# Performance work log

Measured on AMD Instinct MI355X. Metric: run time of the kernel, lower is better.

Reference implementation:

```python
import jax, jax.numpy as jnp
import numpy as np

N = 100_000      # nodes
E = 1_600_000    # directed edges (before self-loops)
F_IN = 256       # input node features
H = 128          # hidden_dim
HEADS = 2
C_HEAD = H // HEADS  # 64, GATConv out_channels per head
G = 128          # graphs in batch
NCLS = 10
NEG_SLOPE = 0.2  # PyG GATConv default


def setup_inputs() -> dict:
    key = jax.random.key(0)
    ks = jax.random.split(key, 20)
    p = lambda k, shape: (jax.random.normal(k, shape, jnp.float32) * 0.05)
    x = jax.random.normal(ks[0], (N, F_IN), jnp.float32)
    edge_index = jax.random.randint(ks[1], (2, E), 0, N, dtype=jnp.int64)
    batch = jnp.sort(jax.random.randint(ks[2], (N,), 0, G, dtype=jnp.int64))
    return dict(
        x=x, edge_index=edge_index, batch=batch,
        pre_w=p(ks[3], (F_IN, H)), pre_b=p(ks[4], (H,)),
        w1=p(ks[5], (H, H)), asrc1=p(ks[6], (HEADS, C_HEAD)), adst1=p(ks[7], (HEADS, C_HEAD)), b1=p(ks[8], (H,)),
        w2=p(ks[9], (H, H)), asrc2=p(ks[10], (HEADS, C_HEAD)), adst2=p(ks[11], (HEADS, C_HEAD)), b2=p(ks[12], (H,)),
        post_w1=p(ks[13], (H, H)), post_b1=p(ks[14], (H,)),
        post_w2=p(ks[15], (H, NCLS)), post_b2=p(ks[16], (NCLS,)),
    )


def _gat_conv(h_in, w, a_src, a_dst, b, src, dst):
    # h: [N, heads, c]
    h = (h_in @ w).reshape(N, HEADS, C_HEAD)
    alpha_src = jnp.sum(h * a_src, axis=-1)  # [N, heads]
    alpha_dst = jnp.sum(h * a_dst, axis=-1)  # [N, heads]
    e = jax.nn.leaky_relu(alpha_src[src] + alpha_dst[dst], NEG_SLOPE)  # [E+N, heads]
    # numerically stable softmax over incoming edges of each destination node
    m = jax.ops.segment_max(e, dst, num_segments=N)
    ex = jnp.exp(e - m[dst])
    denom = jax.ops.segment_sum(ex, dst, num_segments=N)
    alpha = ex / denom[dst]                                           # [E+N, heads]
    out = jax.ops.segment_sum(h[src] * alpha[:, :, None], dst, num_segments=N)
    return out.reshape(N, H) + b  # concat heads + bias


def reference(x, edge_index, batch, pre_w, pre_b,
              w1, asrc1, adst1, b1, w2, asrc2, adst2, b2,
              post_w1, post_b1, post_w2, post_b2):
    # PyG GATConv default add_self_loops=True
    loop = jnp.arange(N, dtype=edge_index.dtype)
    src = jnp.concatenate([edge_index[0], loop])
    dst = jnp.concatenate([edge_index[1], loop])

    h = jax.nn.relu(x @ pre_w + pre_b)
    reprs = jax.ops.segment_sum(h, batch, num_segments=G)
    h = jax.nn.relu(_gat_conv(h, w1, asrc1, adst1, b1, src, dst))
    reprs = reprs + jax.ops.segment_sum(h, batch, num_segments=G)
    h = jax.nn.relu(_gat_conv(h, w2, asrc2, adst2, b2, src, dst))
    reprs = reprs + jax.ops.segment_sum(h, batch, num_segments=G)
    z = jax.nn.relu(reprs @ post_w1 + post_b1) @ post_w2 + post_b2
    return jax.nn.log_softmax(z, axis=-1)
```

## Files before the change

### kernel.cpp

```cpp
#include <hip/hip_runtime.h>
#include <hip/hip_bf16.h>
#include <math.h>

#define NNODES 100000
#define NEDGES 1600000
#define FIN 256
#define HDIM 128
#define NGRAPH 128
#define NCLS 10
#define NEG 0.2f

#define NBUCK 98
#define EPB 4096
#define EBLK ((NEDGES + EPB - 1) / EPB)

typedef short bf8 __attribute__((ext_vector_type(8)));
typedef float f4 __attribute__((ext_vector_type(4)));

__device__ __forceinline__ float lrelu(float x) { return x > 0.f ? x : NEG * x; }

__device__ __forceinline__ unsigned short f2bf(float f) {
  union { float f; unsigned int u; } v; v.f = f;
  unsigned int r = v.u + 0x7fffu + ((v.u >> 16) & 1u);
  return (unsigned short)(r >> 16);
}
__device__ __forceinline__ float bf_lo(unsigned int p) {
  union { unsigned int u; float f; } v; v.u = p << 16; return v.f;
}
__device__ __forceinline__ float bf_hi(unsigned int p) {
  union { unsigned int u; float f; } v; v.u = p & 0xffff0000u; return v.f;
}

__global__ __launch_bounds__(256) void convert_transpose(const float* __restrict__ w,
                                                         unsigned short* __restrict__ wt,
                                                         int K) {
  int i = blockIdx.x * 256 + threadIdx.x;
  if (i >= K * 128) return;
  int k = i >> 7, n = i & 127;
  wt[n * K + k] = f2bf(w[(size_t)k * 128 + n]);
}

__global__ __launch_bounds__(256) void gemm_mfma(const float* __restrict__ A,
                                                 const unsigned short* __restrict__ Bt,
                                                 const float* __restrict__ bias,
                                                 float* __restrict__ C,
                                                 unsigned int* __restrict__ Cp,
                                                 const float* __restrict__ a_src,
                                                 const float* __restrict__ a_dst,
                                                 float* __restrict__ o_as,
                                                 float* __restrict__ o_ad,
                                                 int M, int K, int dorelu) {
  __shared__ bf8 As[512];
  __shared__ bf8 Bs[512];
  int tid = threadIdx.x;
  int wv = tid >> 6, lane = tid & 63;
  int quad = lane >> 4, m16 = lane & 15;
  int row0 = blockIdx.x * 128;

  f4 acc[2][8];
#pragma unroll
  for (int a = 0; a < 2; ++a)
#pragma unroll
    for (int b = 0; b < 8; ++b) acc[a][b] = (f4){0.f, 0.f, 0.f, 0.f};

  for (int kb = 0; kb < K; kb += 32) {
    __syncthreads();
#pragma unroll
    for (int bb = 0; bb < 2; ++bb) {
      int b = tid + bb * 256;
      int l = b & 63, mt = b >> 6;
      int row = row0 + mt * 16 + (l & 15);
      if (row > M - 1) row = M - 1;
      const float* src = &A[(size_t)row * K + kb + (l >> 4) * 8];
      float4 x0 = *reinterpret_cast<const float4*>(src);
      float4 x1 = *reinterpret_cast<const float4*>(src + 4);
      bf8 v;
      v[0] = (short)f2bf(x0.x); v[1] = (short)f2bf(x0.y);
      v[2] = (short)f2bf(x0.z); v[3] = (short)f2bf(x0.w);
      v[4] = (short)f2bf(x1.x); v[5] = (short)f2bf(x1.y);
      v[6] = (short)f2bf(x1.z); v[7] = (short)f2bf(x1.w);
      As[b] = v;
    }
#pragma unroll
    for (int bb = 0; bb < 2; ++bb) {
      int b = tid + bb * 256;
      int l = b & 63, tn = b >> 6;
      int n = tn * 16 + (l & 15);
      Bs[b] = *reinterpret_cast<const bf8*>(&Bt[(size_t)n * K + kb + (l >> 4) * 8]);
    }
    __syncthreads();
    bf8 af0 = As[(wv * 2 + 0) * 64 + lane];
    bf8 af1 = As[(wv * 2 + 1) * 64 + lane];
#pragma unroll
    for (int tn = 0; tn < 8; ++tn) {
      bf8 bfm = Bs[tn * 64 + lane];
      acc[0][tn] = __builtin_amdgcn_mfma_f32_16x16x32_bf16(af0, bfm, acc[0][tn], 0, 0, 0);
      acc[1][tn] = __builtin_amdgcn_mfma_f32_16x16x32_bf16(af1, bfm, acc[1][tn], 0, 0, 0);
    }
  }

  if (Cp) {
    if (a_src) {
      float aS[8], aD[8];
#pragma unroll
      for (int tn = 0; tn < 4; ++tn) {
        aS[tn]     = a_src[tn * 16 + m16];
        aS[tn + 4] = a_src[64 + tn * 16 + m16];
        aD[tn]     = a_dst[tn * 16 + m16];
        aD[tn + 4] = a_dst[64 + tn * 16 + m16];
      }
#pragma unroll
      for (int mt = 0; mt < 2; ++mt)
#pragma unroll
        for (int r = 0; r < 4; ++r) {
          int row = row0 + wv * 32 + mt * 16 + quad * 4 + r;
          float ps0 = 0.f, ps1 = 0.f, pd0 = 0.f, pd1 = 0.f;
#pragma unroll
          for (int tn = 0; tn < 4; ++tn) {
            float v0 = acc[mt][tn][r], v1 = acc[mt][tn + 4][r];
            ps0 = fmaf(v0, aS[tn], ps0);
            ps1 = fmaf(v1, aS[tn + 4], ps1);
            pd0 = fmaf(v0, aD[tn], pd0);
            pd1 = fmaf(v1, aD[tn + 4], pd1);
          }
#pragma unroll
          for (int o = 8; o; o >>= 1) {
            ps0 += __shfl_xor(ps0, o); ps1 += __shfl_xor(ps1, o);
            pd0 += __shfl_xor(pd0, o); pd1 += __shfl_xor(pd1, o);
          }
          if (m16 == 0 && row < M) {
            o_as[2 * row] = ps0; o_as[2 * row + 1] = ps1;
            o_ad[2 * row] = pd0; o_ad[2 * row + 1] = pd1;
          }
        }
    }
#pragma unroll
    for (int mt = 0; mt < 2; ++mt)
#pragma unroll
      for (int tn = 0; tn < 4; ++tn)
#pragma unroll
        for (int r = 0; r < 4; ++r) {
          int row = row0 + wv * 32 + mt * 16 + quad * 4 + r;
          if (row < M) {
            unsigned int p = (unsigned int)f2bf(acc[mt][tn][r]) |
                             ((unsigned int)f2bf(acc[mt][tn + 4][r]) << 16);
            Cp[(size_t)row * 64 + tn * 16 + m16] = p;
          }
        }
  } else {
#pragma unroll
    for (int mt = 0; mt < 2; ++mt)
#pragma unroll
      for (int tn = 0; tn < 8; ++tn) {
        float bv = bias ? bias[tn * 16 + m16] : 0.f;
#pragma unroll
        for (int r = 0; r < 4; ++r) {
          int row = row0 + wv * 32 + mt * 16 + quad * 4 + r;
          if (row < M) {
            float v = acc[mt][tn][r] + bv;
            if (dorelu) v = fmaxf(v, 0.f);
            C[(size_t)row * 128 + tn * 16 + m16] = v;
          }
        }
      }
  }
}

__global__ void find_starts(const int* __restrict__ batch, int* __restrict__ gstart) {
  int g = threadIdx.x;
  if (g > NGRAPH) return;
  if (g == NGRAPH) { gstart[g] = NNODES; return; }
  int lo = 0, hi = NNODES;
  while (lo < hi) { int mid = (lo + hi) >> 1; if (batch[mid] < g) lo = mid + 1; else hi = mid; }
  gstart[g] = lo;
}

__global__ __launch_bounds__(256) void bin_count(const int* __restrict__ edst,
                                                 int* __restrict__ blockHist) {
  __shared__ int hist[NBUCK];
  int t = threadIdx.x, blk = blockIdx.x;
  if (t < NBUCK) hist[t] = 0;
  __syncthreads();
  int e0 = blk * EPB;
#pragma unroll
  for (int it = 0; it < EPB / 256; ++it) {
    int e = e0 + it * 256 + t;
    if (e < NEDGES) atomicAdd(&hist[((unsigned)edst[e]) >> 10], 1);
  }
  __syncthreads();
  if (t < NBUCK) blockHist[blk * NBUCK + t] = hist[t];
}

__global__ __launch_bounds__(512) void colscan(const int* __restrict__ blockHist,
                                               int* __restrict__ blockBaseCol,
                                               int* __restrict__ bucket_total) {
  __shared__ int s[512];
  int b = blockIdx.x, t = threadIdx.x;
  int v = (t < EBLK) ? blockHist[t * NBUCK + b] : 0;
  s[t] = v;
  __syncthreads();
  for (int off = 1; off < 512; off <<= 1) {
    int u = (t >= off) ? s[t - off] : 0;
    __syncthreads();
    s[t] += u;
    __syncthreads();
  }
  if (t < EBLK) blockBaseCol[b * EBLK + t] = s[t] - v;
  if (t == 511) bucket_total[b] = s[511];
}

__global__ __launch_bounds__(128) void bscan(const int* __restrict__ bucket_total,
                                             int* __restrict__ bucket_ptr) {
  __shared__ int s[128];
  int t = threadIdx.x;
  int v = (t < NBUCK) ? bucket_total[t] : 0;
  s[t] = v;
  __syncthreads();
  for (int off = 1; off < 128; off <<= 1) {
    int u = (t >= off) ? s[t - off] : 0;
    __syncthreads();
    s[t] += u;
    __syncthreads();
  }
  if (t < NBUCK) bucket_ptr[t] = s[t] - v;
  if (t == 127) bucket_ptr[NBUCK] = s[127];
}

__global__ __launch_bounds__(512) void bin_place(const int* __restrict__ esrc,
                                                 const int* __restrict__ edst,
                                                 const int* __restrict__ blockBaseCol,
                                                 const int* __restrict__ bucket_ptr,
                                                 uint2* __restrict__ stagingG) {
  __shared__ int hist[NBUCK + 1], lbase[NBUCK + 1], lcur[NBUCK + 1], cbase[NBUCK];
  __shared__ int tmp[128];
  __shared__ uint2 st[EPB];
  int t = threadIdx.x, blk = blockIdx.x;
  if (t < NBUCK + 1) hist[t] = 0;
  __syncthreads();
  int e0 = blk * EPB;
#pragma unroll
  for (int it = 0; it < EPB / 512; ++it) {
    int e = e0 + it * 512 + t;
    int b = NBUCK;
    if (e < NEDGES) b = ((unsigned)edst[e]) >> 10;
    atomicAdd(&hist[b], 1);
  }
  __syncthreads();
  if (t < 128) tmp[t] = (t < NBUCK + 1) ? hist[t] : 0;
  __syncthreads();
  for (int off = 1; off < 128; off <<= 1) {
    int u = 0;
    if (t < 128 && t >= off) u = tmp[t - off];
    __syncthreads();
    if (t < 128) tmp[t] += u;
    __syncthreads();
  }
  if (t < NBUCK + 1) { int ex = tmp[t] - hist[t]; lbase[t] = ex; lcur[t] = ex; }
  if (t < NBUCK) cbase[t] = bucket_ptr[t] + blockBaseCol[t * EBLK + blk];
  __syncthreads();
#pragma unroll
  for (int it = 0; it < EPB / 512; ++it) {
    int e = e0 + it * 512 + t;
    unsigned s = 0, d = 0xFFFFFFFFu;
    if (e < NEDGES) { s = (unsigned)esrc[e]; d = (unsigned)edst[e]; }
    int b = (d == 0xFFFFFFFFu) ? NBUCK : (int)(d >> 10);
    int slot = atomicAdd(&lcur[b], 1);
    st[slot] = make_uint2(s, d);
  }
  __syncthreads();
  for (int i = t; i < EPB; i += 512) {
    uint2 ed = st[i];
    if (ed.y == 0xFFFFFFFFu) continue;
    int b = (int)(ed.y >> 10);
    stagingG[cbase[b] + (i - lbase[b])] = ed;
  }
}

__global__ __launch_bounds__(1024) void bucket_deg(const uint2* __restrict__ stagingG,
                                                   const int* __restrict__ bucket_ptr,
                                                   int* __restrict__ deg) {
  __shared__ int dl[1024];
  int b = blockIdx.x, t = threadIdx.x;
  dl[t] = 0;
  __syncthreads();
  int s0 = bucket_ptr[b], s1 = bucket_ptr[b + 1];
  for (int j = s0 + t; j < s1; j += 1024)
    atomicAdd(&dl[stagingG[j].y & 1023], 1);
  __syncthreads();
  int n = (b << 10) + t;
  if (n < NNODES) deg[n] = dl[t];
}

__global__ __launch_bounds__(256) void scan_block(const int* __restrict__ deg,
                                                  int* __restrict__ incl,
                                                  int* __restrict__ blocksum) {
  __shared__ int s[256];
  int tid = threadIdx.x;
  int i = blockIdx.x * 256 + tid;
  s[tid] = (i < NNODES) ? deg[i] : 0;
  __syncthreads();
  for (int off = 1; off < 256; off <<= 1) {
    int t = (tid >= off) ? s[tid - off] : 0;
    __syncthreads();
    s[tid] += t;
    __syncthreads();
  }
  if (i < NNODES) incl[i] = s[tid];
  if (tid == 255) blocksum[blockIdx.x] = s[255];
}

__global__ void scan_offsets(int* blocksum, int nb) {
  if (threadIdx.x == 0 && blockIdx.x == 0) {
    int run = 0;
    for (int b = 0; b < nb; ++b) { int t = blocksum[b]; blocksum[b] = run; run += t; }
  }
}

__global__ __launch_bounds__(256) void finalize_csr(const int* __restrict__ deg,
                                                    const int* __restrict__ incl,
                                                    const int* __restrict__ blocksum,
                                                    int* __restrict__ row_ptr) {
  int i = blockIdx.x * 256 + threadIdx.x;
  if (i >= NNODES) return;
  int tot = incl[i] + blocksum[i >> 8];
  row_ptr[i] = tot - deg[i];
  if (i == NNODES - 1) row_ptr[NNODES] = tot;
}

__global__ __launch_bounds__(1024) void bucket_csr(const uint2* __restrict__ stagingG,
                                                   const int* __restrict__ bucket_ptr,
                                                   const int* __restrict__ row_ptr,
                                                   int* __restrict__ colv) {
  __shared__ int cur[1024];
  int b = blockIdx.x, t = threadIdx.x;
  int n = (b << 10) + t;
  cur[t] = (n < NNODES) ? row_ptr[n] : 0;
  __syncthreads();
  int s0 = bucket_ptr[b], s1 = bucket_ptr[b + 1];
  for (int j = s0 + t; j < s1; j += 1024) {
    uint2 e = stagingG[j];
    int pos = atomicAdd(&cur[e.y & 1023], 1);
    colv[pos] = (int)e.x;
  }
}

template<int T>
__device__ __forceinline__ void gather_T(const unsigned int* __restrict__ hwb,
                                         int lane, int sl, float w0l, float w1l,
                                         float& acc0, float& acc1) {
#pragma unroll
  for (int t = 0; t < T; ++t) {
    int s = __builtin_amdgcn_readlane(sl, t);
    float w0 = __uint_as_float(__builtin_amdgcn_readlane(__float_as_uint(w0l), t));
    float w1 = __uint_as_float(__builtin_amdgcn_readlane(__float_as_uint(w1l), t));
    unsigned q = hwb[(size_t)s * 64 + lane];
    acc0 = fmaf(w0, bf_lo(q), acc0);
    acc1 = fmaf(w1, bf_hi(q), acc1);
  }
}

__global__ __launch_bounds__(256) void aggregate(const unsigned int* __restrict__ hwb,
                                                 const float* __restrict__ a_s,
                                                 const float* __restrict__ a_d,
                                                 const int* __restrict__ row_ptr,
                                                 const int* __restrict__ colv,
                                                 const float* __restrict__ bias,
                                                 float* __restrict__ out) {
  int i = (blockIdx.x * 256 + threadIdx.x) >> 6;
  int lane = threadIdx.x & 63;
  if (i >= NNODES) return;
  float ad0 = a_d[2 * i], ad1 = a_d[2 * i + 1];
  float es0 = lrelu(a_s[2 * i] + ad0), es1 = lrelu(a_s[2 * i + 1] + ad1);
  int start = row_ptr[i], end = row_ptr[i + 1];
  int deg = end - start;

  int sl = 0; float e0l = -1e30f, e1l = -1e30f;
  if (lane < deg) {
    sl = colv[start + lane];
    float2 av = *reinterpret_cast<const float2*>(&a_s[2 * sl]);
    e0l = lrelu(av.x + ad0); e1l = lrelu(av.y + ad1);
  }
  float m0 = fmaxf(es0, e0l), m1 = fmaxf(es1, e1l);
  for (int j = start + 64 + lane; j < end; j += 64) {
    int s = colv[j];
    float2 av = *reinterpret_cast<const float2*>(&a_s[2 * s]);
    m0 = fmaxf(m0, lrelu(av.x + ad0));
    m1 = fmaxf(m1, lrelu(av.y + ad1));
  }
  for (int o = 32; o; o >>= 1) {
    m0 = fmaxf(m0, __shfl_xor(m0, o));
    m1 = fmaxf(m1, __shfl_xor(m1, o));
  }
  float w0l = lane < deg ? __expf(e0l - m0) : 0.f;
  float w1l = lane < deg ? __expf(e1l - m1) : 0.f;
  float d0 = w0l, d1 = w1l;
  for (int o = 32; o; o >>= 1) { d0 += __shfl_xor(d0, o); d1 += __shfl_xor(d1, o); }
  float ws0 = __expf(es0 - m0), ws1 = __expf(es1 - m1);
  float den0 = d0 + ws0, den1 = d1 + ws1;

  unsigned int ps = hwb[(size_t)i * 64 + lane];
  float acc0 = ws0 * bf_lo(ps), acc1 = ws1 * bf_hi(ps);
  int dmin = deg < 64 ? deg : 64;
  switch ((dmin + 7) >> 3) {
    case 1: gather_T<8 >(hwb, lane, sl, w0l, w1l, acc0, acc1); break;
    case 2: gather_T<16>(hwb, lane, sl, w0l, w1l, acc0, acc1); break;
    case 3: gather_T<24>(hwb, lane, sl, w0l, w1l, acc0, acc1); break;
    case 4: gather_T<32>(hwb, lane, sl, w0l, w1l, acc0, acc1); break;
    case 5: gather_T<40>(hwb, lane, sl, w0l, w1l, acc0, acc1); break;
    case 6: gather_T<48>(hwb, lane, sl, w0l, w1l, acc0, acc1); break;
    case 7: gather_T<56>(hwb, lane, sl, w0l, w1l, acc0, acc1); break;
    case 8: gather_T<64>(hwb, lane, sl, w0l, w1l, acc0, acc1); break;
    default: break;
  }
  for (int j = start + 64; j < end; ++j) {
    int s = colv[j];
    float2 av = *reinterpret_cast<const float2*>(&a_s[2 * s]);
    float w0 = __expf(lrelu(av.x + ad0) - m0);
    float w1 = __expf(lrelu(av.y + ad1) - m1);
    den0 += w0; den1 += w1;
    unsigned int q = hwb[(size_t)s * 64 + lane];
    acc0 = fmaf(w0, bf_lo(q), acc0);
    acc1 = fmaf(w1, bf_hi(q), acc1);
  }
  out[(size_t)i * 128 + lane]      = fmaxf(acc0 / den0 + bias[lane], 0.f);
  out[(size_t)i * 128 + 64 + lane] = fmaxf(acc1 / den1 + bias[64 + lane], 0.f);
}

#define SEG_CHUNK 128
__global__ __launch_bounds__(128) void seg_sum_fast(const float* __restrict__ h,
                                                    const int* __restrict__ batch,
                                                    const int* __restrict__ gstart,
                                                    float* __restrict__ reprs) {
  int n0 = blockIdx.x * SEG_CHUNK;
  if (n0 >= NNODES) return;
  int nend = n0 + SEG_CHUNK; if (nend > NNODES) nend = NNODES;
  int tid = threadIdx.x;
  int r = n0;
  while (r < nend) {
    int g = batch[r];
    int segend = gstart[g + 1]; if (segend > nend) segend = nend;
    float a0 = 0.f, a1 = 0.f, a2 = 0.f, a3 = 0.f;
    for (; r + 3 < segend; r += 4) {
      a0 += h[(size_t)r * 128 + tid];
      a1 += h[(size_t)(r + 1) * 128 + tid];
      a2 += h[(size_t)(r + 2) * 128 + tid];
      a3 += h[(size_t)(r + 3) * 128 + tid];
    }
    for (; r < segend; ++r) a0 += h[(size_t)r * 128 + tid];
    atomicAdd(&reprs[g * 128 + tid], (a0 + a1) + (a2 + a3));
  }
}

__global__ __launch_bounds__(128) void head_kernel(const float* __restrict__ reprs,
                                                   const float* __restrict__ pw1,
                                                   const float* __restrict__ pb1,
                                                   const float* __restrict__ pw2,
                                                   const float* __restrict__ pb2,
                                                   float* __restrict__ out) {
  __shared__ float r[128], t1[128], z[NCLS];
  int g = blockIdx.x, tid = threadIdx.x;
  r[tid] = reprs[g * 128 + tid];
  __syncthreads();
  float acc = pb1[tid];
  for (int k = 0; k < 128; ++k) acc = fmaf(r[k], pw1[k * 128 + tid], acc);
  t1[tid] = fmaxf(acc, 0.f);
  __syncthreads();
  if (tid < NCLS) {
    float zz = pb2[tid];
    for (int k = 0; k < 128; ++k) zz = fmaf(t1[k], pw2[k * NCLS + tid], zz);
    z[tid] = zz;
  }
  __syncthreads();
  if (tid == 0) {
    float mx = -1e30f;
    for (int c = 0; c < NCLS; ++c) mx = fmaxf(mx, z[c]);
    float s = 0.f;
    for (int c = 0; c < NCLS; ++c) s += expf(z[c] - mx);
    float ls = logf(s) + mx;
    for (int c = 0; c < NCLS; ++c) out[g * NCLS + c] = z[c] - ls;
  }
}

extern "C" void kernel_launch(void* const* d_in, const int* in_sizes, int n_in,
                              void* d_out, int out_size, void* d_ws, size_t ws_size,
                              hipStream_t stream) {
  const float* x     = (const float*)d_in[0];
  const int*   eidx  = (const int*)d_in[1];
  const int*   batch = (const int*)d_in[2];
  const float* pre_w = (const float*)d_in[3];
  const float* pre_b = (const float*)d_in[4];
  const float* w1    = (const float*)d_in[5];
  const float* asrc1 = (const float*)d_in[6];
  const float* adst1 = (const float*)d_in[7];
  const float* b1    = (const float*)d_in[8];
  const float* w2    = (const float*)d_in[9];
  const float* asrc2 = (const float*)d_in[10];
  const float* adst2 = (const float*)d_in[11];
  const float* b2    = (const float*)d_in[12];
  const float* pw1   = (const float*)d_in[13];
  const float* pb1   = (const float*)d_in[14];
  const float* pw2   = (const float*)d_in[15];
  const float* pb2   = (const float*)d_in[16];
  float* out = (float*)d_out;

  const int* esrc = eidx;
  const int* edst = eidx + NEDGES;

  char* wsp = (char*)d_ws;
  size_t off = 0;
  auto alloc = [&](size_t bytes) -> void* {
    void* p = wsp + off;
    off += (bytes + 255) & ~(size_t)255;
    return p;
  };
  float* h          = (float*)alloc((size_t)NNODES * 128 * 4);
  unsigned int* hwb = (unsigned int*)alloc((size_t)NNODES * 64 * 4);
  float* a_s        = (float*)alloc((size_t)NNODES * 2 * 4);
  float* a_d        = (float*)alloc((size_t)NNODES * 2 * 4);
  float* reprs      = (float*)alloc((size_t)NGRAPH * 128 * 4);
  int* gstart       = (int*)alloc((NGRAPH + 1) * 4);
  int* deg          = (int*)alloc((size_t)NNODES * 4);
  int* incl         = (int*)alloc((size_t)NNODES * 4);
  int* row_ptr      = (int*)alloc(((size_t)NNODES + 1) * 4);
  int* colv         = (int*)alloc((size_t)NEDGES * 4);
  int* blocksum     = (int*)alloc(512 * 4);
  unsigned short* wt_pre = (unsigned short*)alloc((size_t)128 * FIN * 2);
  unsigned short* wt1    = (unsigned short*)alloc((size_t)128 * HDIM * 2);
  unsigned short* wt2    = (unsigned short*)alloc((size_t)128 * HDIM * 2);
  int* blockHist    = (int*)alloc((size_t)EBLK * NBUCK * 4);
  int* blockBaseCol = (int*)alloc((size_t)NBUCK * EBLK * 4);
  int* bucket_total = (int*)alloc(NBUCK * 4);
  int* bucket_ptr   = (int*)alloc((NBUCK + 1) * 4);
  uint2* stagingG   = (uint2*)alloc((size_t)NEDGES * 8);

  int nb = (NNODES + 255) / 256;
  int wb = NNODES / 4;
  int sb = (NNODES + SEG_CHUNK - 1) / SEG_CHUNK;
  int gb = (NNODES + 127) / 128;

  convert_transpose<<<(FIN * 128 + 255) / 256, 256, 0, stream>>>(pre_w, wt_pre, FIN);
  convert_transpose<<<(HDIM * 128 + 255) / 256, 256, 0, stream>>>(w1, wt1, HDIM);
  convert_transpose<<<(HDIM * 128 + 255) / 256, 256, 0, stream>>>(w2, wt2, HDIM);

  hipMemsetAsync(reprs, 0, (size_t)NGRAPH * 128 * 4, stream);
  find_starts<<<1, 256, 0, stream>>>(batch, gstart);

  bin_count<<<EBLK, 256, 0, stream>>>(edst, blockHist);
  colscan<<<NBUCK, 512, 0, stream>>>(blockHist, blockBaseCol, bucket_total);
  bscan<<<1, 128, 0, stream>>>(bucket_total, bucket_ptr);
  bin_place<<<EBLK, 512, 0, stream>>>(esrc, edst, blockBaseCol, bucket_ptr, stagingG);
  bucket_deg<<<NBUCK, 1024, 0, stream>>>(stagingG, bucket_ptr, deg);
  scan_block<<<nb, 256, 0, stream>>>(deg, incl, blocksum);
  scan_offsets<<<1, 64, 0, stream>>>(blocksum, nb);
  finalize_csr<<<nb, 256, 0, stream>>>(deg, incl, blocksum, row_ptr);
  bucket_csr<<<NBUCK, 1024, 0, stream>>>(stagingG, bucket_ptr, row_ptr, colv);

  gemm_mfma<<<gb, 256, 0, stream>>>(x, wt_pre, pre_b, h, nullptr,
                                    nullptr, nullptr, nullptr, nullptr, NNODES, FIN, 1);
  seg_sum_fast<<<sb, 128, 0, stream>>>(h, batch, gstart, reprs);

  gemm_mfma<<<gb, 256, 0, stream>>>(h, wt1, nullptr, nullptr, hwb,
                                    asrc1, adst1, a_s, a_d, NNODES, HDIM, 0);
  aggregate<<<wb, 256, 0, stream>>>(hwb, a_s, a_d, row_ptr, colv, b1, h);
  seg_sum_fast<<<sb, 128, 0, stream>>>(h, batch, gstart, reprs);

  gemm_mfma<<<gb, 256, 0, stream>>>(h, wt2, nullptr, nullptr, hwb,
                                    asrc2, adst2, a_s, a_d, NNODES, HDIM, 0);
  aggregate<<<wb, 256, 0, stream>>>(hwb, a_s, a_d, row_ptr, colv, b2, h);
  seg_sum_fast<<<sb, 128, 0, stream>>>(h, batch, gstart, reprs);

  head_kernel<<<NGRAPH, 128, 0, stream>>>(reprs, pw1, pb1, pw2, pb2, out);
}
```

Baseline: 572.9 us.

## Gather four edges per wavefront step with 16-byte loads in GAT aggregate

```diff
diff --git a/kernel.cpp b/kernel.cpp
--- a/kernel.cpp
+++ b/kernel.cpp
@@ -345,17 +345,21 @@
 }
 
 template<int T>
-__device__ __forceinline__ void gather_T(const unsigned int* __restrict__ hwb,
-                                         int lane, int sl, float w0l, float w1l,
-                                         float& acc0, float& acc1) {
-#pragma unroll
-  for (int t = 0; t < T; ++t) {
-    int s = __builtin_amdgcn_readlane(sl, t);
-    float w0 = __uint_as_float(__builtin_amdgcn_readlane(__float_as_uint(w0l), t));
-    float w1 = __uint_as_float(__builtin_amdgcn_readlane(__float_as_uint(w1l), t));
-    unsigned q = hwb[(size_t)s * 64 + lane];
-    acc0 = fmaf(w0, bf_lo(q), acc0);
-    acc1 = fmaf(w1, bf_hi(q), acc1);
+__device__ __forceinline__ void gather4(const unsigned int* __restrict__ hwb,
+                                        const int* __restrict__ rowsW,
+                                        const float2* __restrict__ wW,
+                                        int grp, int cg4,
+                                        float* A0, float* A1) {
+#pragma unroll
+  for (int t = 0; t < T; t += 4) {
+    int e = t + grp;
+    int row = rowsW[e];
+    float2 w = wW[e];
+    uint4 q = *reinterpret_cast<const uint4*>(&hwb[(size_t)row * 64 + cg4]);
+    A0[0] = fmaf(w.x, bf_lo(q.x), A0[0]); A1[0] = fmaf(w.y, bf_hi(q.x), A1[0]);
+    A0[1] = fmaf(w.x, bf_lo(q.y), A0[1]); A1[1] = fmaf(w.y, bf_hi(q.y), A1[1]);
+    A0[2] = fmaf(w.x, bf_lo(q.z), A0[2]); A1[2] = fmaf(w.y, bf_hi(q.z), A1[2]);
+    A0[3] = fmaf(w.x, bf_lo(q.w), A0[3]); A1[3] = fmaf(w.y, bf_hi(q.w), A1[3]);
   }
 }
 
@@ -366,9 +370,14 @@
                                                  const int* __restrict__ colv,
                                                  const float* __restrict__ bias,
                                                  float* __restrict__ out) {
-  int i = (blockIdx.x * 256 + threadIdx.x) >> 6;
-  int lane = threadIdx.x & 63;
+  __shared__ int   rowsS[4][64];
+  __shared__ float2 wS[4][64];
+  int tid = threadIdx.x;
+  int wv = tid >> 6, lane = tid & 63;
+  int i = (blockIdx.x * 256 + tid) >> 6;
   if (i >= NNODES) return;
+  int grp = lane >> 4, cg4 = (lane & 15) * 4;
+
   float ad0 = a_d[2 * i], ad1 = a_d[2 * i + 1];
   float es0 = lrelu(a_s[2 * i] + ad0), es1 = lrelu(a_s[2 * i + 1] + ad1);
   int start = row_ptr[i], end = row_ptr[i + 1];
@@ -398,32 +407,67 @@
   float ws0 = __expf(es0 - m0), ws1 = __expf(es1 - m1);
   float den0 = d0 + ws0, den1 = d1 + ws1;
 
-  unsigned int ps = hwb[(size_t)i * 64 + lane];
-  float acc0 = ws0 * bf_lo(ps), acc1 = ws1 * bf_hi(ps);
+  rowsS[wv][lane] = sl;
+  wS[wv][lane] = make_float2(w0l, w1l);
+
+  float A0[4] = {0.f, 0.f, 0.f, 0.f}, A1[4] = {0.f, 0.f, 0.f, 0.f};
+  {
+    uint4 qs = *reinterpret_cast<const uint4*>(&hwb[(size_t)i * 64 + cg4]);
+    if (grp == 0) {
+      A0[0] = ws0 * bf_lo(qs.x); A1[0] = ws1 * bf_hi(qs.x);
+      A0[1] = ws0 * bf_lo(qs.y); A1[1] = ws1 * bf_hi(qs.y);
+      A0[2] = ws0 * bf_lo(qs.z); A1[2] = ws1 * bf_hi(qs.z);
+      A0[3] = ws0 * bf_lo(qs.w); A1[3] = ws1 * bf_hi(qs.w);
+    }
+  }
   int dmin = deg < 64 ? deg : 64;
-  switch ((dmin + 7) >> 3) {
-    case 1: gather_T<8 >(hwb, lane, sl, w0l, w1l, acc0, acc1); break;
-    case 2: gather_T<16>(hwb, lane, sl, w0l, w1l, acc0, acc1); break;
-    case 3: gather_T<24>(hwb, lane, sl, w0l, w1l, acc0, acc1); break;
-    case 4: gather_T<32>(hwb, lane, sl, w0l, w1l, acc0, acc1); break;
-    case 5: gather_T<40>(hwb, lane, sl, w0l, w1l, acc0, acc1); break;
-    case 6: gather_T<48>(hwb, lane, sl, w0l, w1l, acc0, acc1); break;
-    case 7: gather_T<56>(hwb, lane, sl, w0l, w1l, acc0, acc1); break;
-    case 8: gather_T<64>(hwb, lane, sl, w0l, w1l, acc0, acc1); break;
+  const int* rowsW = rowsS[wv];
+  const float2* wW = wS[wv];
+  switch ((dmin + 15) >> 4) {
+    case 1: gather4<16>(hwb, rowsW, wW, grp, cg4, A0, A1); break;
+    case 2: gather4<32>(hwb, rowsW, wW, grp, cg4, A0, A1); break;
+    case 3: gather4<48>(hwb, rowsW, wW, grp, cg4, A0, A1); break;
+    case 4: gather4<64>(hwb, rowsW, wW, grp, cg4, A0, A1); break;
     default: break;
   }
-  for (int j = start + 64; j < end; ++j) {
+  float dd0 = 0.f, dd1 = 0.f;
+  for (int j = start + 64 + grp; j < end; j += 4) {
     int s = colv[j];
     float2 av = *reinterpret_cast<const float2*>(&a_s[2 * s]);
     float w0 = __expf(lrelu(av.x + ad0) - m0);
     float w1 = __expf(lrelu(av.y + ad1) - m1);
-    den0 += w0; den1 += w1;
-    unsigned int q = hwb[(size_t)s * 64 + lane];
-    acc0 = fmaf(w0, bf_lo(q), acc0);
-    acc1 = fmaf(w1, bf_hi(q), acc1);
-  }
-  out[(size_t)i * 128 + lane]      = fmaxf(acc0 / den0 + bias[lane], 0.f);
-  out[(size_t)i * 128 + 64 + lane] = fmaxf(acc1 / den1 + bias[64 + lane], 0.f);
+    dd0 += w0; dd1 += w1;
+    uint4 q = *reinterpret_cast<const uint4*>(&hwb[(size_t)s * 64 + cg4]);
+    A0[0] = fmaf(w0, bf_lo(q.x), A0[0]); A1[0] = fmaf(w1, bf_hi(q.x), A1[0]);
+    A0[1] = fmaf(w0, bf_lo(q.y), A0[1]); A1[1] = fmaf(w1, bf_hi(q.y), A1[1]);
+    A0[2] = fmaf(w0, bf_lo(q.z), A0[2]); A1[2] = fmaf(w1, bf_hi(q.z), A1[2]);
+    A0[3] = fmaf(w0, bf_lo(q.w), A0[3]); A1[3] = fmaf(w1, bf_hi(q.w), A1[3]);
+  }
+  if (deg > 64) {
+    dd0 += __shfl_xor(dd0, 16); dd0 += __shfl_xor(dd0, 32);
+    dd1 += __shfl_xor(dd1, 16); dd1 += __shfl_xor(dd1, 32);
+    den0 += dd0; den1 += dd1;
+  }
+#pragma unroll
+  for (int j = 0; j < 4; ++j) {
+    A0[j] += __shfl_xor(A0[j], 16); A0[j] += __shfl_xor(A0[j], 32);
+    A1[j] += __shfl_xor(A1[j], 16); A1[j] += __shfl_xor(A1[j], 32);
+  }
+  if (grp == 0) {
+    float4 o;
+    o.x = fmaxf(A0[0] / den0 + bias[cg4 + 0], 0.f);
+    o.y = fmaxf(A0[1] / den0 + bias[cg4 + 1], 0.f);
+    o.z = fmaxf(A0[2] / den0 + bias[cg4 + 2], 0.f);
+    o.w = fmaxf(A0[3] / den0 + bias[cg4 + 3], 0.f);
+    *reinterpret_cast<float4*>(&out[(size_t)i * 128 + cg4]) = o;
+  } else if (grp == 1) {
+    float4 o;
+    o.x = fmaxf(A1[0] / den1 + bias[64 + cg4 + 0], 0.f);
+    o.y = fmaxf(A1[1] / den1 + bias[64 + cg4 + 1], 0.f);
+    o.z = fmaxf(A1[2] / den1 + bias[64 + cg4 + 2], 0.f);
+    o.w = fmaxf(A1[3] / den1 + bias[64 + cg4 + 3], 0.f);
+    *reinterpret_cast<float4*>(&out[(size_t)i * 128 + 64 + cg4]) = o;
+  }
 }
 
 #define SEG_CHUNK 128
```

Result: slower. 710.0 us (+23.9%).

## Fuse degree count and CSR prefix scan into per-bucket block scan

Applied to the files above, without the earlier changes.

```diff
diff --git a/kernel.cpp b/kernel.cpp
--- a/kernel.cpp
+++ b/kernel.cpp
@@ -276,9 +276,9 @@
   }
 }
 
-__global__ __launch_bounds__(1024) void bucket_deg(const uint2* __restrict__ stagingG,
-                                                   const int* __restrict__ bucket_ptr,
-                                                   int* __restrict__ deg) {
+__global__ __launch_bounds__(1024) void bucket_deg_scan(const uint2* __restrict__ stagingG,
+                                                        const int* __restrict__ bucket_ptr,
+                                                        int* __restrict__ row_ptr) {
   __shared__ int dl[1024];
   int b = blockIdx.x, t = threadIdx.x;
   dl[t] = 0;
@@ -287,44 +287,17 @@
   for (int j = s0 + t; j < s1; j += 1024)
     atomicAdd(&dl[stagingG[j].y & 1023], 1);
   __syncthreads();
+  int myDeg = dl[t];
+  for (int off = 1; off < 1024; off <<= 1) {
+    int u = (t >= off) ? dl[t - off] : 0;
+    __syncthreads();
+    dl[t] += u;
+    __syncthreads();
+  }
+  int excl = dl[t] - myDeg;
   int n = (b << 10) + t;
-  if (n < NNODES) deg[n] = dl[t];
-}
-
-__global__ __launch_bounds__(256) void scan_block(const int* __restrict__ deg,
-                                                  int* __restrict__ incl,
-                                                  int* __restrict__ blocksum) {
-  __shared__ int s[256];
-  int tid = threadIdx.x;
-  int i = blockIdx.x * 256 + tid;
-  s[tid] = (i < NNODES) ? deg[i] : 0;
-  __syncthreads();
-  for (int off = 1; off < 256; off <<= 1) {
-    int t = (tid >= off) ? s[tid - off] : 0;
-    __syncthreads();
-    s[tid] += t;
-    __syncthreads();
-  }
-  if (i < NNODES) incl[i] = s[tid];
-  if (tid == 255) blocksum[blockIdx.x] = s[255];
-}
-
-__global__ void scan_offsets(int* blocksum, int nb) {
-  if (threadIdx.x == 0 && blockIdx.x == 0) {
-    int run = 0;
-    for (int b = 0; b < nb; ++b) { int t = blocksum[b]; blocksum[b] = run; run += t; }
-  }
-}
-
-__global__ __launch_bounds__(256) void finalize_csr(const int* __restrict__ deg,
-                                                    const int* __restrict__ incl,
-                                                    const int* __restrict__ blocksum,
-                                                    int* __restrict__ row_ptr) {
-  int i = blockIdx.x * 256 + threadIdx.x;
-  if (i >= NNODES) return;
-  int tot = incl[i] + blocksum[i >> 8];
-  row_ptr[i] = tot - deg[i];
-  if (i == NNODES - 1) row_ptr[NNODES] = tot;
+  if (n < NNODES) row_ptr[n] = s0 + excl;
+  if (n == NNODES - 1) row_ptr[NNODES] = s0 + excl + myDeg;
 }
 
 __global__ __launch_bounds__(1024) void bucket_csr(const uint2* __restrict__ stagingG,
@@ -519,11 +492,8 @@
   float* a_d        = (float*)alloc((size_t)NNODES * 2 * 4);
   float* reprs      = (float*)alloc((size_t)NGRAPH * 128 * 4);
   int* gstart       = (int*)alloc((NGRAPH + 1) * 4);
-  int* deg          = (int*)alloc((size_t)NNODES * 4);
-  int* incl         = (int*)alloc((size_t)NNODES * 4);
   int* row_ptr      = (int*)alloc(((size_t)NNODES + 1) * 4);
   int* colv         = (int*)alloc((size_t)NEDGES * 4);
-  int* blocksum     = (int*)alloc(512 * 4);
   unsigned short* wt_pre = (unsigned short*)alloc((size_t)128 * FIN * 2);
   unsigned short* wt1    = (unsigned short*)alloc((size_t)128 * HDIM * 2);
   unsigned short* wt2    = (unsigned short*)alloc((size_t)128 * HDIM * 2);
@@ -533,7 +503,6 @@
   int* bucket_ptr   = (int*)alloc((NBUCK + 1) * 4);
   uint2* stagingG   = (uint2*)alloc((size_t)NEDGES * 8);
 
-  int nb = (NNODES + 255) / 256;
   int wb = NNODES / 4;
   int sb = (NNODES + SEG_CHUNK - 1) / SEG_CHUNK;
   int gb = (NNODES + 127) / 128;
@@ -549,10 +518,7 @@
   colscan<<<NBUCK, 512, 0, stream>>>(blockHist, blockBaseCol, bucket_total);
   bscan<<<1, 128, 0, stream>>>(bucket_total, bucket_ptr);
   bin_place<<<EBLK, 512, 0, stream>>>(esrc, edst, blockBaseCol, bucket_ptr, stagingG);
-  bucket_deg<<<NBUCK, 1024, 0, stream>>>(stagingG, bucket_ptr, deg);
-  scan_block<<<nb, 256, 0, stream>>>(deg, incl, blocksum);
-  scan_offsets<<<1, 64, 0, stream>>>(blocksum, nb);
-  finalize_csr<<<nb, 256, 0, stream>>>(deg, incl, blocksum, row_ptr);
+  bucket_deg_scan<<<NBUCK, 1024, 0, stream>>>(stagingG, bucket_ptr, row_ptr);
   bucket_csr<<<NBUCK, 1024, 0, stream>>>(stagingG, bucket_ptr, row_ptr, colv);
 
   gemm_mfma<<<gb, 256, 0, stream>>>(x, wt_pre, pre_b, h, nullptr,
```

Result: faster. 528.2 us (-7.8%).
